# Kernel tuning notes

Measured on AMD Instinct MI355X. Metric: run time of the kernel, lower is better.

Reference implementation:

```python
import jax, jax.numpy as jnp
import numpy as np

ROPE_BASE = 10000.0

def apply_rope(x):
    # x: [B, S, H, Dh]  (rotate-half / NeoX convention)
    B, S, H, Dh = x.shape
    inv_freq = 1.0 / (ROPE_BASE ** (jnp.arange(0, Dh, 2, dtype=jnp.float32) / Dh))  # [Dh/2]
    ang = jnp.arange(S, dtype=jnp.float32)[:, None] * inv_freq[None, :]             # [S, Dh/2]
    cos = jnp.cos(ang)[None, :, None, :].astype(x.dtype)  # [1,S,1,Dh/2]
    sin = jnp.sin(ang)[None, :, None, :].astype(x.dtype)
    x1, x2 = jnp.split(x, 2, axis=-1)
    return jnp.concatenate([x1 * cos - x2 * sin, x1 * sin + x2 * cos], axis=-1)

def setup_inputs() -> dict:
    key = jax.random.key(0)
    k1, k2, k3 = jax.random.split(key, 3)
    B, S, D = 2, 2048, 1024
    x = jax.random.normal(k1, (B, S, D), dtype=jnp.float32)
    attn_mask = jnp.ones((B, S), dtype=bool)
    qkv_w = jax.random.normal(k2, (D, 3 * D), dtype=jnp.float32) * (1.0 / np.sqrt(D))
    out_w = jax.random.normal(k3, (D, D), dtype=jnp.float32) * (1.0 / np.sqrt(D))
    return {"x": x, "qkv_w": qkv_w, "out_w": out_w, "attn_mask": attn_mask, "is_causal": 1}

def reference(x, qkv_w, out_w, attn_mask, is_causal):
    B, S, D = x.shape
    H = 16
    Dh = D // H
    qkv = x @ qkv_w                                  # [B,S,3D]
    q, k, v = jnp.split(qkv, 3, axis=-1)
    q = apply_rope(q.reshape(B, S, H, Dh))           # [B,S,H,Dh]
    k = apply_rope(k.reshape(B, S, H, Dh))
    v = v.reshape(B, S, H, Dh)
    scale = 1.0 / np.sqrt(Dh)
    att = jnp.einsum('bqhd,bkhd->bhqk', q, k) * scale  # [B,H,S,S]
    if is_causal:
        mask = jnp.tril(jnp.ones((S, S), dtype=bool))[None, None]
    else:
        mask = attn_mask[:, None, None, :]             # [B,1,1,S]
    att = jnp.where(mask, att, jnp.finfo(att.dtype).min)
    p = jax.nn.softmax(att, axis=-1)
    y = jnp.einsum('bhqk,bkhd->bqhd', p, v).reshape(B, S, D)
    return y @ out_w
```

## Files before the change

kernel.cpp:

```cpp
#include <hip/hip_runtime.h>
#include <hip/hip_bf16.h>

#define BB 2
#define SS 2048
#define DD 1024
#define HH 16
#define N3 3072

typedef __attribute__((ext_vector_type(8))) short bf16x8;
typedef __attribute__((ext_vector_type(4))) float f32x4;

__device__ __forceinline__ float b2f(unsigned short u) {
    return __uint_as_float(((unsigned int)u) << 16);
}
__device__ __forceinline__ unsigned short f2b(float f) {
    unsigned int x = __float_as_uint(f);
    x += 0x7fffu + ((x >> 16) & 1u);
    return (unsigned short)(x >> 16);
}
__device__ __forceinline__ unsigned int pack2bf(float a, float b) {
    __hip_bfloat162 h = __float22bfloat162_rn(make_float2(a, b));
    return *(unsigned int*)&h;
}
__device__ __forceinline__ void storeC(float* p, float v) { *p = v; }
__device__ __forceinline__ void storeC(unsigned short* p, float v) { *p = f2b(v); }

__device__ __forceinline__ void gload_lds16(const void* g, void* l) {
    __builtin_amdgcn_global_load_lds(
        (__attribute__((address_space(1))) void*)g,
        (__attribute__((address_space(3))) void*)l, 16, 0, 0);
}

__global__ __launch_bounds__(256) void sincos_tab(float2* __restrict__ tab) {
    int i = blockIdx.x * 256 + threadIdx.x;
    int t = i & 31;
    int s = i >> 5;
    float inv = powf(10000.0f, -(float)t * (1.0f / 32.0f));
    float sn, c;
    sincosf((float)s * inv, &sn, &c);
    tab[i] = make_float2(c, sn);
}

__global__ __launch_bounds__(256) void cast_f32_bf16(
    const float* __restrict__ src, unsigned short* __restrict__ dst)
{
    int i = (blockIdx.x * 256 + threadIdx.x) * 4;
    float4 f = *(const float4*)(src + i);
    uint2 o;
    o.x = pack2bf(f.x, f.y);
    o.y = pack2bf(f.z, f.w);
    *(uint2*)(dst + i) = o;
}

__global__ __launch_bounds__(256) void cast_transpose(
    const float* __restrict__ src, unsigned short* __restrict__ dst,
    int R, int C)
{
    __shared__ unsigned short tile[64][66];
    const int t = threadIdx.x;
    const int c0 = blockIdx.x * 64, r0 = blockIdx.y * 64;
    const int lr = t >> 4;
    const int lc = (t & 15) * 4;
    #pragma unroll
    for (int i = 0; i < 4; ++i) {
        float4 f = *(const float4*)(src + (size_t)(r0 + lr + i * 16) * C + c0 + lc);
        tile[lr + i * 16][lc + 0] = f2b(f.x);
        tile[lr + i * 16][lc + 1] = f2b(f.y);
        tile[lr + i * 16][lc + 2] = f2b(f.z);
        tile[lr + i * 16][lc + 3] = f2b(f.w);
    }
    __syncthreads();
    #pragma unroll
    for (int i = 0; i < 4; ++i) {
        const int wr = lr + i * 16;
        ushort4 o;
        o.x = tile[lc + 0][wr];
        o.y = tile[lc + 1][wr];
        o.z = tile[lc + 2][wr];
        o.w = tile[lc + 3][wr];
        *(ushort4*)(dst + (size_t)(c0 + wr) * R + r0 + lc) = o;
    }
}

template <typename OutT, int TN>
__global__ __launch_bounds__(256) void gemm_mfma(
    const unsigned short* __restrict__ A,
    const unsigned short* __restrict__ Bt,
    OutT* __restrict__ C,
    int M, int N, int K)
{
    constexpr int NI = TN / 32;
    constexpr int NB = TN / 64;
    __shared__ unsigned short Al[128 * 32];
    __shared__ unsigned short Bl[TN * 32];
    const int tid  = threadIdx.x;
    const int wave = tid >> 6;
    const int lane = tid & 63;
    const int quad = lane >> 4;
    const int l16  = lane & 15;
    const int m0 = blockIdx.y * 128;
    const int n0 = blockIdx.x * TN;
    const int wm = (wave >> 1) * 64;
    const int wn = (wave & 1) * (TN / 2);

    const int srowA = wave * 32 + (lane >> 2);
    const int srowB = wave * (16 * NB) + (lane >> 2);
    const int scol  = (lane & 3) * 8;
    const unsigned short* gA = A  + (size_t)(m0 + srowA) * K + scol;
    const unsigned short* gB = Bt + (size_t)(n0 + srowB) * K + scol;

    f32x4 acc[4][NI];
    #pragma unroll
    for (int mi = 0; mi < 4; ++mi)
        #pragma unroll
        for (int ni = 0; ni < NI; ++ni)
            acc[mi][ni] = (f32x4){0.f, 0.f, 0.f, 0.f};

    for (int k0 = 0; k0 < K; k0 += 32) {
        __syncthreads();
        #pragma unroll
        for (int i = 0; i < 2; ++i)
            gload_lds16(gA + (size_t)i * 16 * K + k0, Al + (wave * 2 + i) * 512);
        #pragma unroll
        for (int i = 0; i < NB; ++i)
            gload_lds16(gB + (size_t)i * 16 * K + k0, Bl + (wave * NB + i) * 512);
        __syncthreads();

        bf16x8 af[4], bfr[NI];
        #pragma unroll
        for (int mi = 0; mi < 4; ++mi)
            af[mi] = *(const bf16x8*)&Al[(wm + mi * 16 + l16) * 32 + quad * 8];
        #pragma unroll
        for (int ni = 0; ni < NI; ++ni)
            bfr[ni] = *(const bf16x8*)&Bl[(wn + ni * 16 + l16) * 32 + quad * 8];
        #pragma unroll
        for (int mi = 0; mi < 4; ++mi)
            #pragma unroll
            for (int ni = 0; ni < NI; ++ni)
                acc[mi][ni] = __builtin_amdgcn_mfma_f32_16x16x32_bf16(
                    af[mi], bfr[ni], acc[mi][ni], 0, 0, 0);
    }

    #pragma unroll
    for (int mi = 0; mi < 4; ++mi) {
        #pragma unroll
        for (int r = 0; r < 4; ++r) {
            const size_t base = (size_t)(m0 + wm + mi * 16 + quad * 4 + r) * N + n0 + wn;
            #pragma unroll
            for (int ni = 0; ni < NI; ++ni)
                storeC(&C[base + ni * 16 + l16], acc[mi][ni][r]);
        }
    }
}

__global__ __launch_bounds__(256) void rope_split(
    const unsigned short* __restrict__ qkv,
    const float2* __restrict__ tab,
    unsigned short* __restrict__ qo,
    unsigned short* __restrict__ ko,
    unsigned short* __restrict__ vt)
{
    __shared__ unsigned short Vtile[64][72];

    const int s0 = blockIdx.x * 64;
    const int h  = blockIdx.y;
    const int b  = blockIdx.z;
    const int tid = threadIdx.x;
    const int sl = tid >> 2;
    const int qu = tid & 3;
    const size_t bh = (size_t)b * HH + h;

    const unsigned short* row = qkv + (size_t)(b * SS + s0 + sl) * N3 + h * 64;

    uint4 a0 = *(const uint4*)(row + qu * 8);
    uint4 a1 = *(const uint4*)(row + 32 + qu * 8);
    uint4 b0 = *(const uint4*)(row + DD + qu * 8);
    uint4 b1 = *(const uint4*)(row + DD + 32 + qu * 8);
    uint4 c0 = *(const uint4*)(row + 2 * DD + qu * 8);
    uint4 c1 = *(const uint4*)(row + 2 * DD + 32 + qu * 8);

    float2 cs[8];
    {
        const float4* tp = (const float4*)(tab + (size_t)(s0 + sl) * 32 + qu * 8);
        #pragma unroll
        for (int i = 0; i < 4; ++i) {
            float4 f = tp[i];
            cs[2 * i]     = make_float2(f.x, f.y);
            cs[2 * i + 1] = make_float2(f.z, f.w);
        }
    }

    const unsigned short* pa0 = (const unsigned short*)&a0;
    const unsigned short* pa1 = (const unsigned short*)&a1;
    const unsigned short* pb0 = (const unsigned short*)&b0;
    const unsigned short* pb1 = (const unsigned short*)&b1;
    const unsigned short* pc0 = (const unsigned short*)&c0;
    const unsigned short* pc1 = (const unsigned short*)&c1;

    unsigned short oq1[8], oq2[8], ok1[8], ok2[8];
    #pragma unroll
    for (int j = 0; j < 8; ++j) {
        float c = cs[j].x, sn = cs[j].y;
        float q1 = b2f(pa0[j]), q2 = b2f(pa1[j]);
        float k1 = b2f(pb0[j]), k2 = b2f(pb1[j]);
        oq1[j] = f2b(q1 * c - q2 * sn);
        oq2[j] = f2b(q1 * sn + q2 * c);
        ok1[j] = f2b(k1 * c - k2 * sn);
        ok2[j] = f2b(k1 * sn + k2 * c);
        Vtile[qu * 8 + j][sl]      = pc0[j];
        Vtile[32 + qu * 8 + j][sl] = pc1[j];
    }
    const size_t qoff = (bh * SS + s0 + sl) * 64;
    *(uint4*)(qo + qoff + qu * 8)      = *(const uint4*)oq1;
    *(uint4*)(qo + qoff + 32 + qu * 8) = *(const uint4*)oq2;
    *(uint4*)(ko + qoff + qu * 8)      = *(const uint4*)ok1;
    *(uint4*)(ko + qoff + 32 + qu * 8) = *(const uint4*)ok2;

    __syncthreads();

    const int dr = tid >> 2;
    const int ch = tid & 3;
    uint4 t0 = *(const uint4*)&Vtile[dr][ch * 16];
    uint4 t1 = *(const uint4*)&Vtile[dr][ch * 16 + 8];
    unsigned short* vrow = vt + (bh * 64 + dr) * SS + s0 + ch * 16;
    *(uint4*)vrow       = t0;
    *(uint4*)(vrow + 8) = t1;
}

__device__ __forceinline__ void attn_step(
    const unsigned short* __restrict__ Kb,
    const unsigned short* __restrict__ Vb,
    unsigned short* __restrict__ PqW,
    const bf16x8 qf0, const bf16x8 qf1,
    f32x4 O[4], float& m_run, float& l_run,
    bool diag, const unsigned char* mrow,
    int kt, int quad, int l16, int csw, int qg)
{
    const float SC = 0.18033688011112042f;

    f32x4 Sf[4];
    #pragma unroll
    for (int st = 0; st < 4; ++st) {
        const unsigned short* kr = &Kb[(st * 16 + l16) * 64];
        bf16x8 kf0 = *(const bf16x8*)(kr + csw * 8);
        bf16x8 kf1 = *(const bf16x8*)(kr + (csw ^ 4) * 8);
        f32x4 s = (f32x4){0.f, 0.f, 0.f, 0.f};
        s = __builtin_amdgcn_mfma_f32_16x16x32_bf16(kf0, qf0, s, 0, 0, 0);
        s = __builtin_amdgcn_mfma_f32_16x16x32_bf16(kf1, qf1, s, 0, 0, 0);
        #pragma unroll
        for (int r = 0; r < 4; ++r) s[r] *= SC;
        Sf[st] = s;
    }

    if (diag) {
        #pragma unroll
        for (int st = 0; st < 4; ++st) {
            const int kb0 = kt * 64 + st * 16 + quad * 4;
            #pragma unroll
            for (int r = 0; r < 4; ++r)
                if (kb0 + r > qg) Sf[st][r] = -1e30f;
        }
    } else if (mrow) {
        #pragma unroll
        for (int st = 0; st < 4; ++st) {
            uchar4 mv = *(const uchar4*)(mrow + st * 16 + quad * 4);
            if (!mv.x) Sf[st][0] = -1e30f;
            if (!mv.y) Sf[st][1] = -1e30f;
            if (!mv.z) Sf[st][2] = -1e30f;
            if (!mv.w) Sf[st][3] = -1e30f;
        }
    }

    float mx = Sf[0][0];
    #pragma unroll
    for (int st = 0; st < 4; ++st)
        #pragma unroll
        for (int r = 0; r < 4; ++r) mx = fmaxf(mx, Sf[st][r]);
    mx = fmaxf(mx, __shfl_xor(mx, 16));
    mx = fmaxf(mx, __shfl_xor(mx, 32));
    const float mnew = fmaxf(m_run, mx);
    const float alpha = exp2f(m_run - mnew);
    m_run = mnew;

    float lsum = 0.f;
    #pragma unroll
    for (int st = 0; st < 4; ++st)
        #pragma unroll
        for (int r = 0; r < 4; ++r) {
            float p = exp2f(Sf[st][r] - mnew);
            Sf[st][r] = p;
            lsum += p;
        }
    lsum += __shfl_xor(lsum, 16);
    lsum += __shfl_xor(lsum, 32);
    l_run = l_run * alpha + lsum;

    #pragma unroll
    for (int st = 0; st < 4; ++st)
        #pragma unroll
        for (int r = 0; r < 4; ++r) O[st][r] *= alpha;

    #pragma unroll
    for (int st = 0; st < 4; ++st) {
        uint2 pk;
        pk.x = pack2bf(Sf[st][0], Sf[st][1]);
        pk.y = pack2bf(Sf[st][2], Sf[st][3]);
        *(uint2*)&PqW[l16 * 72 + st * 16 + quad * 4] = pk;
    }
    bf16x8 pf0 = *(const bf16x8*)&PqW[l16 * 72 + quad * 8];
    bf16x8 pf1 = *(const bf16x8*)&PqW[l16 * 72 + 32 + quad * 8];

    #pragma unroll
    for (int st = 0; st < 4; ++st) {
        const unsigned short* vr = &Vb[(st * 16 + l16) * 64];
        bf16x8 vf0 = *(const bf16x8*)(vr + csw * 8);
        bf16x8 vf1 = *(const bf16x8*)(vr + (csw ^ 4) * 8);
        O[st] = __builtin_amdgcn_mfma_f32_16x16x32_bf16(vf0, pf0, O[st], 0, 0, 0);
        O[st] = __builtin_amdgcn_mfma_f32_16x16x32_bf16(vf1, pf1, O[st], 0, 0, 0);
    }
}

__global__ __launch_bounds__(256) void flash_attn(
    const unsigned short* __restrict__ q,
    const unsigned short* __restrict__ k,
    const unsigned short* __restrict__ vt,
    unsigned short* __restrict__ y,
    const int* __restrict__ is_causal,
    const unsigned char* __restrict__ attn_mask)
{
    __shared__ unsigned short Kl[2][64 * 64];
    __shared__ unsigned short Vl[2][64 * 64];
    __shared__ unsigned short Pq[4][16 * 72];

    const int j   = blockIdx.x;
    const int h   = blockIdx.y;
    const int b   = blockIdx.z;
    const int tid = threadIdx.x;
    const int wave = tid >> 6;
    const int lane = tid & 63;
    const int quad = lane >> 4;
    const int l16  = lane & 15;

    const size_t bh = (size_t)b * HH + h;
    const bool causal = (is_causal[0] != 0);
    const int NT = SS / 64;
    const int tA = j, tB = NT - 1 - j;
    const int ntrips = causal ? (tB + 1) : NT;

    const unsigned short* qrowA = q + (bh * SS + tA * 64 + wave * 16 + l16) * 64;
    const unsigned short* qrowB = q + (bh * SS + tB * 64 + wave * 16 + l16) * 64;
    const bf16x8 qfA0 = *(const bf16x8*)(qrowA + quad * 8);
    const bf16x8 qfA1 = *(const bf16x8*)(qrowA + 32 + quad * 8);
    const bf16x8 qfB0 = *(const bf16x8*)(qrowB + quad * 8);
    const bf16x8 qfB1 = *(const bf16x8*)(qrowB + 32 + quad * 8);

    const unsigned short* kbase  = k  + bh * SS * 64;
    const unsigned short* vtbase = vt + bh * 64 * SS;

    const int Rl  = lane >> 3;
    const int cph = lane & 7;
    const int csw = quad ^ (l16 & 7);

    f32x4 OA[4], OB[4];
    #pragma unroll
    for (int st = 0; st < 4; ++st) {
        OA[st] = (f32x4){0.f, 0.f, 0.f, 0.f};
        OB[st] = (f32x4){0.f, 0.f, 0.f, 0.f};
    }
    float mA = -1e30f, lA = 0.f, mB = -1e30f, lB = 0.f;

    const int qgA = tA * 64 + wave * 16 + l16;
    const int qgB = tB * 64 + wave * 16 + l16;

    auto stage = [&](int kt) {
        const int buf = kt & 1;
        #pragma unroll
        for (int i = 0; i < 2; ++i) {
            const int jj = wave * 2 + i;
            const int R  = jj * 8 + Rl;
            const int cl = cph ^ (R & 7);
            gload_lds16(kbase + ((size_t)(kt * 64 + R) * 64 + cl * 8),
                        &Kl[buf][jj * 512]);
            gload_lds16(vtbase + ((size_t)R * SS + kt * 64 + cl * 8),
                        &Vl[buf][jj * 512]);
        }
    };

    stage(0);
    for (int kt = 0; kt < ntrips; ++kt) {
        __syncthreads();
        if (kt + 1 < ntrips) stage(kt + 1);

        const unsigned short* Kb = Kl[kt & 1];
        const unsigned short* Vb = Vl[kt & 1];
        const unsigned char* mrow = causal ? nullptr
                                           : (attn_mask + (size_t)b * SS + kt * 64);

        if (!causal || kt <= tA)
            attn_step(Kb, Vb, Pq[wave], qfA0, qfA1, OA, mA, lA,
                      causal && kt == tA, mrow, kt, quad, l16, csw, qgA);
        attn_step(Kb, Vb, Pq[wave], qfB0, qfB1, OB, mB, lB,
                  causal && kt == tB, mrow, kt, quad, l16, csw, qgB);
    }

    const float invA = 1.0f / lA;
    unsigned short* yrowA = y + ((size_t)b * SS + qgA) * DD + h * 64;
    #pragma unroll
    for (int st = 0; st < 4; ++st) {
        uint2 o;
        o.x = pack2bf(OA[st][0] * invA, OA[st][1] * invA);
        o.y = pack2bf(OA[st][2] * invA, OA[st][3] * invA);
        *(uint2*)(yrowA + st * 16 + quad * 4) = o;
    }
    const float invB = 1.0f / lB;
    unsigned short* yrowB = y + ((size_t)b * SS + qgB) * DD + h * 64;
    #pragma unroll
    for (int st = 0; st < 4; ++st) {
        uint2 o;
        o.x = pack2bf(OB[st][0] * invB, OB[st][1] * invB);
        o.y = pack2bf(OB[st][2] * invB, OB[st][3] * invB);
        *(uint2*)(yrowB + st * 16 + quad * 4) = o;
    }
}

extern "C" void kernel_launch(void* const* d_in, const int* in_sizes, int n_in,
                              void* d_out, int out_size, void* d_ws, size_t ws_size,
                              hipStream_t stream) {
    const float* x      = (const float*)d_in[0];
    const float* qkv_w  = (const float*)d_in[1];
    const float* out_w  = (const float*)d_in[2];
    const unsigned char* mask = (const unsigned char*)d_in[3];
    const int*   is_c   = (const int*)d_in[4];
    float* out = (float*)d_out;

    unsigned short* xb  = (unsigned short*)d_ws;
    unsigned short* w1t = xb  + (size_t)4096 * 1024;
    unsigned short* w2t = w1t + (size_t)3072 * 1024;
    unsigned short* qkv = w2t + (size_t)1024 * 1024;
    unsigned short* qb  = qkv + (size_t)4096 * 3072;
    unsigned short* kb  = qb  + (size_t)BB * HH * SS * 64;
    unsigned short* vt  = kb  + (size_t)BB * HH * SS * 64;
    float2* tab = (float2*)(vt + (size_t)BB * HH * SS * 64);
    unsigned short* yb = xb;

    sincos_tab<<<(SS * 32) / 256, 256, 0, stream>>>(tab);
    cast_f32_bf16<<<(4096 * 1024) / 1024, 256, 0, stream>>>(x, xb);
    cast_transpose<<<dim3(N3 / 64, DD / 64), 256, 0, stream>>>(qkv_w, w1t, DD, N3);
    cast_transpose<<<dim3(DD / 64, DD / 64), 256, 0, stream>>>(out_w, w2t, DD, DD);

    gemm_mfma<unsigned short, 128><<<dim3(N3 / 128, 4096 / 128), 256, 0, stream>>>(
        xb, w1t, qkv, 4096, N3, DD);

    rope_split<<<dim3(SS / 64, HH, BB), 256, 0, stream>>>(qkv, tab, qb, kb, vt);

    flash_attn<<<dim3(SS / 128, HH, BB), 256, 0, stream>>>(qb, kb, vt, yb, is_c, mask);

    gemm_mfma<float, 64><<<dim3(DD / 64, 4096 / 128), 256, 0, stream>>>(
        yb, w2t, out, 4096, DD, DD);
}
```

Before: 218.4 us.

## Split attention KV range across two blocks and merge partials in a separate kernel

The flash attention kernel is split into two blocks per query-tile pair. Each block handles half of the KV tiles and writes unnormalized bf16 partial outputs plus per-row running max and sum into a buffer that reuses the qkv workspace. A new merge kernel rescales and combines the two partials into y. This is meant to double the grid and raise CU occupancy. The change also folds the softmax scale into Q during RoPE, removing the per-score multiply, and replaces the padded P staging buffer in LDS with an XOR-swizzled layout. The costs are an extra launch, a round trip of the partials through global memory, and slightly different rounding from scaling Q before its bf16 cast.

```diff
diff --git a/kernel.cpp b/kernel.cpp
--- a/kernel.cpp
+++ b/kernel.cpp
@@ -161,6 +161,7 @@
     unsigned short* __restrict__ vt)
 {
     __shared__ unsigned short Vtile[64][72];
+    const float SC = 0.18033688011112042f;
 
     const int s0 = blockIdx.x * 64;
     const int h  = blockIdx.y;
@@ -203,8 +204,8 @@
         float c = cs[j].x, sn = cs[j].y;
         float q1 = b2f(pa0[j]), q2 = b2f(pa1[j]);
         float k1 = b2f(pb0[j]), k2 = b2f(pb1[j]);
-        oq1[j] = f2b(q1 * c - q2 * sn);
-        oq2[j] = f2b(q1 * sn + q2 * c);
+        oq1[j] = f2b((q1 * c - q2 * sn) * SC);
+        oq2[j] = f2b((q1 * sn + q2 * c) * SC);
         ok1[j] = f2b(k1 * c - k2 * sn);
         ok2[j] = f2b(k1 * sn + k2 * c);
         Vtile[qu * 8 + j][sl]      = pc0[j];
@@ -236,8 +237,6 @@
     bool diag, const unsigned char* mrow,
     int kt, int quad, int l16, int csw, int qg)
 {
-    const float SC = 0.18033688011112042f;
-
     f32x4 Sf[4];
     #pragma unroll
     for (int st = 0; st < 4; ++st) {
@@ -247,8 +246,6 @@
         f32x4 s = (f32x4){0.f, 0.f, 0.f, 0.f};
         s = __builtin_amdgcn_mfma_f32_16x16x32_bf16(kf0, qf0, s, 0, 0, 0);
         s = __builtin_amdgcn_mfma_f32_16x16x32_bf16(kf1, qf1, s, 0, 0, 0);
-        #pragma unroll
-        for (int r = 0; r < 4; ++r) s[r] *= SC;
         Sf[st] = s;
     }
 
@@ -305,10 +302,12 @@
         uint2 pk;
         pk.x = pack2bf(Sf[st][0], Sf[st][1]);
         pk.y = pack2bf(Sf[st][2], Sf[st][3]);
-        *(uint2*)&PqW[l16 * 72 + st * 16 + quad * 4] = pk;
-    }
-    bf16x8 pf0 = *(const bf16x8*)&PqW[l16 * 72 + quad * 8];
-    bf16x8 pf1 = *(const bf16x8*)&PqW[l16 * 72 + 32 + quad * 8];
+        const int c = st * 2 + (quad >> 1);
+        const int p = c ^ (l16 & 7);
+        *(uint2*)&PqW[l16 * 64 + p * 8 + (quad & 1) * 4] = pk;
+    }
+    bf16x8 pf0 = *(const bf16x8*)&PqW[l16 * 64 + csw * 8];
+    bf16x8 pf1 = *(const bf16x8*)&PqW[l16 * 64 + (csw ^ 4) * 8];
 
     #pragma unroll
     for (int st = 0; st < 4; ++st) {
@@ -320,19 +319,22 @@
     }
 }
 
-__global__ __launch_bounds__(256) void flash_attn(
+__global__ __launch_bounds__(256) void flash_part(
     const unsigned short* __restrict__ q,
     const unsigned short* __restrict__ k,
     const unsigned short* __restrict__ vt,
-    unsigned short* __restrict__ y,
+    unsigned short* __restrict__ Opart,
+    float2* __restrict__ ml,
     const int* __restrict__ is_causal,
     const unsigned char* __restrict__ attn_mask)
 {
     __shared__ unsigned short Kl[2][64 * 64];
     __shared__ unsigned short Vl[2][64 * 64];
-    __shared__ unsigned short Pq[4][16 * 72];
-
-    const int j   = blockIdx.x;
+    __shared__ unsigned short Pq[4][16 * 64];
+
+    const int jx  = blockIdx.x;
+    const int j   = jx >> 1;
+    const int half = jx & 1;
     const int h   = blockIdx.y;
     const int b   = blockIdx.z;
     const int tid = threadIdx.x;
@@ -345,7 +347,10 @@
     const bool causal = (is_causal[0] != 0);
     const int NT = SS / 64;
     const int tA = j, tB = NT - 1 - j;
-    const int ntrips = causal ? (tB + 1) : NT;
+    const int n  = causal ? (tB + 1) : NT;
+    const int h1 = (n + 1) >> 1;
+    const int k0 = half ? h1 : 0;
+    const int k1 = half ? n : h1;
 
     const unsigned short* qrowA = q + (bh * SS + tA * 64 + wave * 16 + l16) * 64;
     const unsigned short* qrowB = q + (bh * SS + tB * 64 + wave * 16 + l16) * 64;
@@ -386,10 +391,10 @@
         }
     };
 
-    stage(0);
-    for (int kt = 0; kt < ntrips; ++kt) {
+    if (k0 < k1) stage(k0);
+    for (int kt = k0; kt < k1; ++kt) {
         __syncthreads();
-        if (kt + 1 < ntrips) stage(kt + 1);
+        if (kt + 1 < k1) stage(kt + 1);
 
         const unsigned short* Kb = Kl[kt & 1];
         const unsigned short* Vb = Vl[kt & 1];
@@ -403,24 +408,63 @@
                   causal && kt == tB, mrow, kt, quad, l16, csw, qgB);
     }
 
-    const float invA = 1.0f / lA;
-    unsigned short* yrowA = y + ((size_t)b * SS + qgA) * DD + h * 64;
-    #pragma unroll
-    for (int st = 0; st < 4; ++st) {
-        uint2 o;
-        o.x = pack2bf(OA[st][0] * invA, OA[st][1] * invA);
-        o.y = pack2bf(OA[st][2] * invA, OA[st][3] * invA);
-        *(uint2*)(yrowA + st * 16 + quad * 4) = o;
-    }
-    const float invB = 1.0f / lB;
-    unsigned short* yrowB = y + ((size_t)b * SS + qgB) * DD + h * 64;
-    #pragma unroll
-    for (int st = 0; st < 4; ++st) {
-        uint2 o;
-        o.x = pack2bf(OB[st][0] * invB, OB[st][1] * invB);
-        o.y = pack2bf(OB[st][2] * invB, OB[st][3] * invB);
-        *(uint2*)(yrowB + st * 16 + quad * 4) = o;
-    }
+    auto wpart = [&](int qt, f32x4* O, float m, float l) {
+        const size_t idx = (bh * 32 + qt) * 2 + half;
+        unsigned short* orow = Opart + idx * 4096 + (size_t)(wave * 16 + l16) * 64;
+        #pragma unroll
+        for (int st = 0; st < 4; ++st) {
+            uint2 o;
+            o.x = pack2bf(O[st][0], O[st][1]);
+            o.y = pack2bf(O[st][2], O[st][3]);
+            *(uint2*)(orow + st * 16 + quad * 4) = o;
+        }
+        if (quad == 0) ml[idx * 64 + wave * 16 + l16] = make_float2(m, l);
+    };
+    wpart(tA, OA, mA, lA);
+    wpart(tB, OB, mB, lB);
+}
+
+__global__ __launch_bounds__(256) void attn_merge(
+    const unsigned short* __restrict__ Opart,
+    const float2* __restrict__ ml,
+    unsigned short* __restrict__ y)
+{
+    const int qt = blockIdx.x;
+    const int h  = blockIdx.y;
+    const int b  = blockIdx.z;
+    const size_t bh = (size_t)b * HH + h;
+    const int t  = threadIdx.x;
+    const int qq = t >> 2;
+    const int dg = (t & 3) * 16;
+
+    const size_t base = (bh * 32 + qt) * 2;
+    const float2 ml0 = ml[base * 64 + qq];
+    const float2 ml1 = ml[(base + 1) * 64 + qq];
+    const float m  = fmaxf(ml0.x, ml1.x);
+    const float a0 = exp2f(ml0.x - m);
+    const float a1 = exp2f(ml1.x - m);
+    const float inv = 1.0f / (a0 * ml0.y + a1 * ml1.y);
+    const float s0 = a0 * inv, s1 = a1 * inv;
+
+    const unsigned short* o0 = Opart + base * 4096 + (size_t)qq * 64 + dg;
+    const unsigned short* o1 = Opart + (base + 1) * 4096 + (size_t)qq * 64 + dg;
+    unsigned short* yrow = y + ((size_t)b * SS + qt * 64 + qq) * DD + h * 64 + dg;
+
+    uint4 u0[2], u1[2];
+    u0[0] = *(const uint4*)o0;       u0[1] = *(const uint4*)(o0 + 8);
+    u1[0] = *(const uint4*)o1;       u1[1] = *(const uint4*)(o1 + 8);
+    const unsigned short* p0 = (const unsigned short*)u0;
+    const unsigned short* p1 = (const unsigned short*)u1;
+    uint4 out[1]; unsigned int ov[8];
+    #pragma unroll
+    for (int e = 0; e < 8; ++e) {
+        float v0 = s0 * b2f(p0[2 * e])     + s1 * b2f(p1[2 * e]);
+        float v1 = s0 * b2f(p0[2 * e + 1]) + s1 * b2f(p1[2 * e + 1]);
+        ov[e] = pack2bf(v0, v1);
+    }
+    *(uint4*)yrow       = *(uint4*)&ov[0];
+    *(uint4*)(yrow + 8) = *(uint4*)&ov[4];
+    (void)out;
 }
 
 extern "C" void kernel_launch(void* const* d_in, const int* in_sizes, int n_in,
@@ -442,6 +486,8 @@
     unsigned short* vt  = kb  + (size_t)BB * HH * SS * 64;
     float2* tab = (float2*)(vt + (size_t)BB * HH * SS * 64);
     unsigned short* yb = xb;
+    unsigned short* Opart = qkv;
+    float2* ml = (float2*)(qkv + (size_t)2048 * 4096);
 
     sincos_tab<<<(SS * 32) / 256, 256, 0, stream>>>(tab);
     cast_f32_bf16<<<(4096 * 1024) / 1024, 256, 0, stream>>>(x, xb);
@@ -453,7 +499,10 @@
 
     rope_split<<<dim3(SS / 64, HH, BB), 256, 0, stream>>>(qkv, tab, qb, kb, vt);
 
-    flash_attn<<<dim3(SS / 128, HH, BB), 256, 0, stream>>>(qb, kb, vt, yb, is_c, mask);
+    flash_part<<<dim3(32, HH, BB), 256, 0, stream>>>(
+        qb, kb, vt, Opart, ml, is_c, mask);
+
+    attn_merge<<<dim3(32, HH, BB), 256, 0, stream>>>(Opart, ml, yb);
 
     gemm_mfma<float, 64><<<dim3(DD / 64, 4096 / 128), 256, 0, stream>>>(
         yb, w2t, out, 4096, DD, DD);
```

Measured after the change: 222.8 us. 2.0% more time.

## Restructure flash attention into independent per-wave tiles reading K/V from global

Applied to the files above, without the earlier changes.

The flash attention kernel is replaced by a per-wave version. Each wave owns 32 consecutive query rows and reads K and V fragments straight from global memory, dropping the shared-memory double buffering and the per-tile block barriers. Each K/V fragment is reused across two 16-row query subtiles. The softmax scale is folded into Q during the rope pass, and the P scratch layout in shared memory gains an XOR swizzle. In exchange, the four waves of a block no longer share K/V through shared memory, there is no explicit prefetch of the next tile, and the causal work is no longer balanced by pairing short and long query tiles.

```diff
diff --git a/kernel.cpp b/kernel.cpp
--- a/kernel.cpp
+++ b/kernel.cpp
@@ -161,6 +161,7 @@
     unsigned short* __restrict__ vt)
 {
     __shared__ unsigned short Vtile[64][72];
+    const float SC = 0.18033688011112042f;
 
     const int s0 = blockIdx.x * 64;
     const int h  = blockIdx.y;
@@ -203,8 +204,8 @@
         float c = cs[j].x, sn = cs[j].y;
         float q1 = b2f(pa0[j]), q2 = b2f(pa1[j]);
         float k1 = b2f(pb0[j]), k2 = b2f(pb1[j]);
-        oq1[j] = f2b(q1 * c - q2 * sn);
-        oq2[j] = f2b(q1 * sn + q2 * c);
+        oq1[j] = f2b((q1 * c - q2 * sn) * SC);
+        oq2[j] = f2b((q1 * sn + q2 * c) * SC);
         ok1[j] = f2b(k1 * c - k2 * sn);
         ok2[j] = f2b(k1 * sn + k2 * c);
         Vtile[qu * 8 + j][sl]      = pc0[j];
@@ -227,50 +228,12 @@
     *(uint4*)(vrow + 8) = t1;
 }
 
-__device__ __forceinline__ void attn_step(
-    const unsigned short* __restrict__ Kb,
-    const unsigned short* __restrict__ Vb,
+__device__ __forceinline__ void softmax_pv(
+    f32x4 Sf[4], f32x4 O[4], float& m_run, float& l_run,
+    const bf16x8 vf0[4], const bf16x8 vf1[4],
     unsigned short* __restrict__ PqW,
-    const bf16x8 qf0, const bf16x8 qf1,
-    f32x4 O[4], float& m_run, float& l_run,
-    bool diag, const unsigned char* mrow,
-    int kt, int quad, int l16, int csw, int qg)
-{
-    const float SC = 0.18033688011112042f;
-
-    f32x4 Sf[4];
-    #pragma unroll
-    for (int st = 0; st < 4; ++st) {
-        const unsigned short* kr = &Kb[(st * 16 + l16) * 64];
-        bf16x8 kf0 = *(const bf16x8*)(kr + csw * 8);
-        bf16x8 kf1 = *(const bf16x8*)(kr + (csw ^ 4) * 8);
-        f32x4 s = (f32x4){0.f, 0.f, 0.f, 0.f};
-        s = __builtin_amdgcn_mfma_f32_16x16x32_bf16(kf0, qf0, s, 0, 0, 0);
-        s = __builtin_amdgcn_mfma_f32_16x16x32_bf16(kf1, qf1, s, 0, 0, 0);
-        #pragma unroll
-        for (int r = 0; r < 4; ++r) s[r] *= SC;
-        Sf[st] = s;
-    }
-
-    if (diag) {
-        #pragma unroll
-        for (int st = 0; st < 4; ++st) {
-            const int kb0 = kt * 64 + st * 16 + quad * 4;
-            #pragma unroll
-            for (int r = 0; r < 4; ++r)
-                if (kb0 + r > qg) Sf[st][r] = -1e30f;
-        }
-    } else if (mrow) {
-        #pragma unroll
-        for (int st = 0; st < 4; ++st) {
-            uchar4 mv = *(const uchar4*)(mrow + st * 16 + quad * 4);
-            if (!mv.x) Sf[st][0] = -1e30f;
-            if (!mv.y) Sf[st][1] = -1e30f;
-            if (!mv.z) Sf[st][2] = -1e30f;
-            if (!mv.w) Sf[st][3] = -1e30f;
-        }
-    }
-
+    int quad, int l16, int csw)
+{
     float mx = Sf[0][0];
     #pragma unroll
     for (int st = 0; st < 4; ++st)
@@ -305,22 +268,21 @@
         uint2 pk;
         pk.x = pack2bf(Sf[st][0], Sf[st][1]);
         pk.y = pack2bf(Sf[st][2], Sf[st][3]);
-        *(uint2*)&PqW[l16 * 72 + st * 16 + quad * 4] = pk;
-    }
-    bf16x8 pf0 = *(const bf16x8*)&PqW[l16 * 72 + quad * 8];
-    bf16x8 pf1 = *(const bf16x8*)&PqW[l16 * 72 + 32 + quad * 8];
+        const int c = st * 2 + (quad >> 1);
+        const int p = c ^ (l16 & 7);
+        *(uint2*)&PqW[l16 * 64 + p * 8 + (quad & 1) * 4] = pk;
+    }
+    bf16x8 pf0 = *(const bf16x8*)&PqW[l16 * 64 + csw * 8];
+    bf16x8 pf1 = *(const bf16x8*)&PqW[l16 * 64 + (csw ^ 4) * 8];
 
     #pragma unroll
     for (int st = 0; st < 4; ++st) {
-        const unsigned short* vr = &Vb[(st * 16 + l16) * 64];
-        bf16x8 vf0 = *(const bf16x8*)(vr + csw * 8);
-        bf16x8 vf1 = *(const bf16x8*)(vr + (csw ^ 4) * 8);
-        O[st] = __builtin_amdgcn_mfma_f32_16x16x32_bf16(vf0, pf0, O[st], 0, 0, 0);
-        O[st] = __builtin_amdgcn_mfma_f32_16x16x32_bf16(vf1, pf1, O[st], 0, 0, 0);
-    }
-}
-
-__global__ __launch_bounds__(256) void flash_attn(
+        O[st] = __builtin_amdgcn_mfma_f32_16x16x32_bf16(vf0[st], pf0, O[st], 0, 0, 0);
+        O[st] = __builtin_amdgcn_mfma_f32_16x16x32_bf16(vf1[st], pf1, O[st], 0, 0, 0);
+    }
+}
+
+__global__ __launch_bounds__(256) void flash_wave(
     const unsigned short* __restrict__ q,
     const unsigned short* __restrict__ k,
     const unsigned short* __restrict__ vt,
@@ -328,27 +290,25 @@
     const int* __restrict__ is_causal,
     const unsigned char* __restrict__ attn_mask)
 {
-    __shared__ unsigned short Kl[2][64 * 64];
-    __shared__ unsigned short Vl[2][64 * 64];
-    __shared__ unsigned short Pq[4][16 * 72];
-
-    const int j   = blockIdx.x;
-    const int h   = blockIdx.y;
-    const int b   = blockIdx.z;
-    const int tid = threadIdx.x;
+    __shared__ unsigned short Pq[4][16 * 64];
+
+    const int tid  = threadIdx.x;
     const int wave = tid >> 6;
     const int lane = tid & 63;
     const int quad = lane >> 4;
     const int l16  = lane & 15;
-
+    const int csw  = quad ^ (l16 & 7);
+
+    const int h = blockIdx.y, b = blockIdx.z;
     const size_t bh = (size_t)b * HH + h;
+    const int u = blockIdx.x * 4 + wave;
+    const int qbase = u * 32;
+
     const bool causal = (is_causal[0] != 0);
-    const int NT = SS / 64;
-    const int tA = j, tB = NT - 1 - j;
-    const int ntrips = causal ? (tB + 1) : NT;
-
-    const unsigned short* qrowA = q + (bh * SS + tA * 64 + wave * 16 + l16) * 64;
-    const unsigned short* qrowB = q + (bh * SS + tB * 64 + wave * 16 + l16) * 64;
+    const int ntrips = causal ? ((u + 2) >> 1) : (SS / 64);
+
+    const unsigned short* qrowA = q + (bh * SS + qbase + l16) * 64;
+    const unsigned short* qrowB = qrowA + 16 * 64;
     const bf16x8 qfA0 = *(const bf16x8*)(qrowA + quad * 8);
     const bf16x8 qfA1 = *(const bf16x8*)(qrowA + 32 + quad * 8);
     const bf16x8 qfB0 = *(const bf16x8*)(qrowB + quad * 8);
@@ -357,10 +317,6 @@
     const unsigned short* kbase  = k  + bh * SS * 64;
     const unsigned short* vtbase = vt + bh * 64 * SS;
 
-    const int Rl  = lane >> 3;
-    const int cph = lane & 7;
-    const int csw = quad ^ (l16 & 7);
-
     f32x4 OA[4], OB[4];
     #pragma unroll
     for (int st = 0; st < 4; ++st) {
@@ -368,39 +324,63 @@
         OB[st] = (f32x4){0.f, 0.f, 0.f, 0.f};
     }
     float mA = -1e30f, lA = 0.f, mB = -1e30f, lB = 0.f;
-
-    const int qgA = tA * 64 + wave * 16 + l16;
-    const int qgB = tB * 64 + wave * 16 + l16;
-
-    auto stage = [&](int kt) {
-        const int buf = kt & 1;
-        #pragma unroll
-        for (int i = 0; i < 2; ++i) {
-            const int jj = wave * 2 + i;
-            const int R  = jj * 8 + Rl;
-            const int cl = cph ^ (R & 7);
-            gload_lds16(kbase + ((size_t)(kt * 64 + R) * 64 + cl * 8),
-                        &Kl[buf][jj * 512]);
-            gload_lds16(vtbase + ((size_t)R * SS + kt * 64 + cl * 8),
-                        &Vl[buf][jj * 512]);
-        }
-    };
-
-    stage(0);
+    const int qgA = qbase + l16;
+    const int qgB = qbase + 16 + l16;
+    unsigned short* PqW = Pq[wave];
+
     for (int kt = 0; kt < ntrips; ++kt) {
-        __syncthreads();
-        if (kt + 1 < ntrips) stage(kt + 1);
-
-        const unsigned short* Kb = Kl[kt & 1];
-        const unsigned short* Vb = Vl[kt & 1];
-        const unsigned char* mrow = causal ? nullptr
-                                           : (attn_mask + (size_t)b * SS + kt * 64);
-
-        if (!causal || kt <= tA)
-            attn_step(Kb, Vb, Pq[wave], qfA0, qfA1, OA, mA, lA,
-                      causal && kt == tA, mrow, kt, quad, l16, csw, qgA);
-        attn_step(Kb, Vb, Pq[wave], qfB0, qfB1, OB, mB, lB,
-                  causal && kt == tB, mrow, kt, quad, l16, csw, qgB);
+        const int kk0 = kt * 64;
+
+        f32x4 SA[4], SB[4];
+        #pragma unroll
+        for (int st = 0; st < 4; ++st) {
+            const unsigned short* kr = kbase + (size_t)(kk0 + st * 16 + l16) * 64;
+            bf16x8 kf0 = *(const bf16x8*)(kr + quad * 8);
+            bf16x8 kf1 = *(const bf16x8*)(kr + 32 + quad * 8);
+            f32x4 s = (f32x4){0.f, 0.f, 0.f, 0.f};
+            s = __builtin_amdgcn_mfma_f32_16x16x32_bf16(kf0, qfA0, s, 0, 0, 0);
+            s = __builtin_amdgcn_mfma_f32_16x16x32_bf16(kf1, qfA1, s, 0, 0, 0);
+            SA[st] = s;
+            f32x4 t2 = (f32x4){0.f, 0.f, 0.f, 0.f};
+            t2 = __builtin_amdgcn_mfma_f32_16x16x32_bf16(kf0, qfB0, t2, 0, 0, 0);
+            t2 = __builtin_amdgcn_mfma_f32_16x16x32_bf16(kf1, qfB1, t2, 0, 0, 0);
+            SB[st] = t2;
+        }
+
+        bf16x8 vf0[4], vf1[4];
+        #pragma unroll
+        for (int st = 0; st < 4; ++st) {
+            const unsigned short* vr = vtbase + (size_t)(st * 16 + l16) * SS + kk0;
+            vf0[st] = *(const bf16x8*)(vr + quad * 8);
+            vf1[st] = *(const bf16x8*)(vr + 32 + quad * 8);
+        }
+
+        if (causal) {
+            if (kt == ntrips - 1) {
+                #pragma unroll
+                for (int st = 0; st < 4; ++st) {
+                    const int kb0 = kk0 + st * 16 + quad * 4;
+                    #pragma unroll
+                    for (int r = 0; r < 4; ++r) {
+                        if (kb0 + r > qgA) SA[st][r] = -1e30f;
+                        if (kb0 + r > qgB) SB[st][r] = -1e30f;
+                    }
+                }
+            }
+        } else {
+            #pragma unroll
+            for (int st = 0; st < 4; ++st) {
+                uchar4 mv = *(const uchar4*)(attn_mask + (size_t)b * SS + kk0
+                                             + st * 16 + quad * 4);
+                if (!mv.x) { SA[st][0] = -1e30f; SB[st][0] = -1e30f; }
+                if (!mv.y) { SA[st][1] = -1e30f; SB[st][1] = -1e30f; }
+                if (!mv.z) { SA[st][2] = -1e30f; SB[st][2] = -1e30f; }
+                if (!mv.w) { SA[st][3] = -1e30f; SB[st][3] = -1e30f; }
+            }
+        }
+
+        softmax_pv(SA, OA, mA, lA, vf0, vf1, PqW, quad, l16, csw);
+        softmax_pv(SB, OB, mB, lB, vf0, vf1, PqW, quad, l16, csw);
     }
 
     const float invA = 1.0f / lA;
@@ -453,7 +433,7 @@
 
     rope_split<<<dim3(SS / 64, HH, BB), 256, 0, stream>>>(qkv, tab, qb, kb, vt);
 
-    flash_attn<<<dim3(SS / 128, HH, BB), 256, 0, stream>>>(qb, kb, vt, yb, is_c, mask);
+    flash_wave<<<dim3(16, HH, BB), 256, 0, stream>>>(qb, kb, vt, yb, is_c, mask);
 
     gemm_mfma<float, 64><<<dim3(DD / 64, 4096 / 128), 256, 0, stream>>>(
         yb, w2t, out, 4096, DD, DD);
```

New measurement: 272.1 us. +24.5%, slower.
